# Kernel tuning notes

Hardware: AMD Instinct MI355X
Metric: run time of the kernel (lower is better)

Reference implementation:

```python
import jax, jax.numpy as jnp
import numpy as np

B, N_UNITS, SEQ, H = 4, 1024, 2048, 8
D_HEAD = N_UNITS // H
SCALE = 1.0 / D_HEAD ** 0.5


def setup_inputs() -> dict:
    key = jax.random.key(0)
    k1, k2, k3 = jax.random.split(key, 3)
    x = jax.random.normal(k1, (B, N_UNITS, SEQ), dtype=jnp.float32)
    # conv1x1 weights, bias=False; scaled like typical init
    W_qkv = jax.random.normal(k2, (3 * N_UNITS, N_UNITS), dtype=jnp.float32) * (1.0 / N_UNITS ** 0.5)
    W_out = jax.random.normal(k3, (N_UNITS, N_UNITS), dtype=jnp.float32) * (1.0 / N_UNITS ** 0.5)
    return {"x": x, "W_qkv": W_qkv, "W_out": W_out}


def reference(x, W_qkv, W_out):
    # x: (B, n_units, S). Conv1x1 == per-position linear along channel dim.
    qkv = jnp.einsum('oc,bcs->bos', W_qkv, x)          # (B, 3*n_units, S)
    Q, K, V = jnp.split(qkv, 3, axis=1)                # each (B, n_units, S)
    # torch.chunk along channels into h heads == reshape (B, h, d_head, S)
    Q = Q.reshape(B, H, D_HEAD, SEQ)
    K = K.reshape(B, H, D_HEAD, SEQ)
    V = V.reshape(B, H, D_HEAD, SEQ)
    # scores: Q^T K * scale  (NO softmax in original module; mask unused)
    A = jnp.einsum('bhdq,bhdk->bhqk', Q, K) * SCALE    # (B, h, S, S)
    # aggregation: sum_k A[q,k] * V[d,k]  (original does broadcast mul+sum)
    C = jnp.einsum('bhqk,bhdk->bhdq', A, V)            # (B, h, d_head, S)
    C = C.reshape(B, N_UNITS, SEQ)
    out = jnp.einsum('oc,bcs->bos', W_out, C)          # (B, n_units, S)
    return out
```

## Files before the change

### kernel.cpp

```cpp
#include <hip/hip_runtime.h>
#include <hip/hip_bf16.h>
#include <stdint.h>

using bf16 = __hip_bfloat16;

typedef __bf16 bf16x8 __attribute__((ext_vector_type(8)));
typedef float  f32x4  __attribute__((ext_vector_type(4)));

constexpr int Bc = 4, Hh = 8, Dh = 128, S = 2048, Cn = 1024, O3 = 3072;
constexpr float SCALE = 0.08838834764831845f;

#define GLDS16(gp, lp)                                               \
  __builtin_amdgcn_global_load_lds(                                  \
      (const __attribute__((address_space(1))) void*)(gp),           \
      (__attribute__((address_space(3))) void*)(lp), 16, 0, 0)

#define WAITVM(N) asm volatile("s_waitcnt vmcnt(" #N ")" ::: "memory")
#define BAR()                                  \
  do {                                         \
    asm volatile("" ::: "memory");             \
    __builtin_amdgcn_s_barrier();              \
    asm volatile("" ::: "memory");             \
  } while (0)

__device__ __forceinline__ void gemm_bt_core(
    const bf16* __restrict__ Abase, int lda,
    const bf16* __restrict__ Bbase, int ldb,
    int kIters, f32x4 (&acc)[4][4])
{
  alignas(16) __shared__ bf16 As[128 * 32];
  alignas(16) __shared__ bf16 Bs[128 * 32];
  const int t    = threadIdx.x;
  const int lane = t & 63;
  const int quad = lane >> 4, r16 = lane & 15;
  const int wave = t >> 6;
  const int wm = (wave & 1) * 64, wn = (wave >> 1) * 64;
  const int lrow = lane >> 2;
  const int lk   = (lane & 3) * 8;

  const long aOff0 = (long)(wave * 32 + lrow) * lda + lk;
  const long aOff1 = aOff0 + 16l * lda;
  const long bOff0 = (long)(wave * 32 + lrow) * ldb + lk;
  const long bOff1 = bOff0 + 16l * ldb;
  bf16* aL0 = &As[(wave * 32) * 32];
  bf16* aL1 = &As[(wave * 32 + 16) * 32];
  bf16* bL0 = &Bs[(wave * 32) * 32];
  bf16* bL1 = &Bs[(wave * 32 + 16) * 32];

#pragma unroll
  for (int i = 0; i < 4; i++)
#pragma unroll
    for (int j = 0; j < 4; j++) acc[i][j] = {0.f, 0.f, 0.f, 0.f};

  for (int ks = 0; ks < kIters; ++ks) {
    const int k0 = ks * 32;
    __syncthreads();
    GLDS16(Abase + k0 + aOff0, aL0);
    GLDS16(Abase + k0 + aOff1, aL1);
    GLDS16(Bbase + k0 + bOff0, bL0);
    GLDS16(Bbase + k0 + bOff1, bL1);
    __syncthreads();
    bf16x8 af[4], bfr[4];
#pragma unroll
    for (int i = 0; i < 4; i++)
      af[i] = *(const bf16x8*)&As[(wm + i * 16 + r16) * 32 + quad * 8];
#pragma unroll
    for (int j = 0; j < 4; j++)
      bfr[j] = *(const bf16x8*)&Bs[(wn + j * 16 + r16) * 32 + quad * 8];
#pragma unroll
    for (int i = 0; i < 4; i++)
#pragma unroll
      for (int j = 0; j < 4; j++)
        acc[i][j] = __builtin_amdgcn_mfma_f32_16x16x32_bf16(af[i], bfr[j], acc[i][j], 0, 0, 0);
  }
}

__device__ __forceinline__ void store_bf16_tile(
    f32x4 (&acc)[4][4], bf16* __restrict__ Cp, int ldc)
{
  const int t = threadIdx.x;
  const int lane = t & 63;
  const int quad = lane >> 4, r16 = lane & 15;
  const int wave = t >> 6;
  const int wm = (wave & 1) * 64, wn = (wave >> 1) * 64;
#pragma unroll
  for (int i = 0; i < 4; i++)
#pragma unroll
    for (int j = 0; j < 4; j++)
#pragma unroll
      for (int r = 0; r < 4; r++) {
        const int row = wm + i * 16 + quad * 4 + r;
        const int col = wn + j * 16 + r16;
        Cp[(long)row * ldc + col] = __float2bfloat16(acc[i][j][r]);
      }
}

__device__ __forceinline__ void store_f32_tile(
    f32x4 (&acc)[4][4], float* __restrict__ Cp, int ldc)
{
  const int t = threadIdx.x;
  const int lane = t & 63;
  const int quad = lane >> 4, r16 = lane & 15;
  const int wave = t >> 6;
  const int wm = (wave & 1) * 64, wn = (wave >> 1) * 64;
#pragma unroll
  for (int i = 0; i < 4; i++)
#pragma unroll
    for (int j = 0; j < 4; j++)
#pragma unroll
      for (int r = 0; r < 4; r++) {
        const int row = wm + i * 16 + quad * 4 + r;
        const int col = wn + j * 16 + r16;
        Cp[(long)row * ldc + col] = acc[i][j][r];
      }
}

__device__ __forceinline__ void kv_body(
    const bf16* __restrict__ WkvB, const bf16* __restrict__ xT,
    bf16* __restrict__ KV, bf16* sm, int orig)
{
  constexpr int NT = Cn / 32;
  const int mt = orig >> 5;
  const int nt = ((orig & 7) << 2) | ((orig >> 3) & 3);
  const int m0 = mt * 256;

  const int tid  = threadIdx.x;
  const int lane = tid & 63;
  const int w    = tid >> 6;
  const int quad = lane >> 4, r16 = lane & 15;
  const int wm = (w >> 2) * 128;
  const int wn = (w & 3) * 64;

  const int srow = w * 16 + (lane >> 2);
  const int cx   = (lane & 3) ^ ((lane >> 3) & 3);
  const bf16* Ag = WkvB + (long)(m0 + srow) * Cn + cx * 8;
  const bf16* Bg = xT + (long)((long)nt * 256 + srow) * Cn + cx * 8;
  const int ldsW = w * 512;

#define KV8_STAGE_A(tt)                                                   \
  do {                                                                    \
    const int k0_ = (tt) * 32, bb_ = ((tt) & 3) * 16384;                  \
    GLDS16(Ag + k0_,             &sm[bb_ + ldsW]);                        \
    GLDS16(Ag + 128l * Cn + k0_, &sm[bb_ + 4096 + ldsW]);                 \
  } while (0)
#define KV8_STAGE_B(tt)                                                   \
  do {                                                                    \
    const int k0_ = (tt) * 32, bb_ = ((tt) & 3) * 16384;                  \
    GLDS16(Bg + k0_,             &sm[bb_ + 8192 + ldsW]);                 \
    GLDS16(Bg + 128l * Cn + k0_, &sm[bb_ + 8192 + 4096 + ldsW]);          \
  } while (0)

  const int sc8 = (quad ^ ((r16 >> 1) & 3)) * 8;

  f32x4 acc[8][4];
#pragma unroll
  for (int m = 0; m < 8; m++)
#pragma unroll
    for (int n = 0; n < 4; n++) acc[m][n] = {0.f, 0.f, 0.f, 0.f};

  KV8_STAGE_A(0); KV8_STAGE_B(0);
  KV8_STAGE_A(1); KV8_STAGE_B(1);
  KV8_STAGE_A(2); KV8_STAGE_B(2);
  WAITVM(8);
  BAR();

  bf16x8 af0[4], bfr0[4], af1[4];
  {
    const bf16* Ab = &sm[0];
    const bf16* Bb = Ab + 8192;
#pragma unroll
    for (int n = 0; n < 4; n++)
      bfr0[n] = *(const bf16x8*)&Bb[(wn + n * 16 + r16) * 32 + sc8];
#pragma unroll
    for (int m = 0; m < 4; m++)
      af0[m] = *(const bf16x8*)&Ab[(wm + m * 16 + r16) * 32 + sc8];
  }

#pragma unroll 4
  for (int tt = 0; tt < NT; ++tt) {
    const bf16* Ab = &sm[(tt & 3) * 16384];

    BAR();
    if (tt + 3 < NT) { KV8_STAGE_A(tt + 3); KV8_STAGE_B(tt + 3); }
#pragma unroll
    for (int m = 0; m < 4; m++)
      af1[m] = *(const bf16x8*)&Ab[(wm + (m + 4) * 16 + r16) * 32 + sc8];
    __builtin_amdgcn_s_setprio(1);
#pragma unroll
    for (int m = 0; m < 4; m++)
#pragma unroll
      for (int n = 0; n < 4; n++)
        acc[m][n] = __builtin_amdgcn_mfma_f32_16x16x32_bf16(af0[m], bfr0[n], acc[m][n], 0, 0, 0);
    __builtin_amdgcn_s_setprio(0);

    if (tt <= NT - 4)      { WAITVM(8); }
    else if (tt == NT - 3) { WAITVM(4); }
    else if (tt == NT - 2) { WAITVM(0); }
    BAR();

    __builtin_amdgcn_s_setprio(1);
#pragma unroll
    for (int m = 0; m < 4; m++)
#pragma unroll
      for (int n = 0; n < 4; n++)
        acc[m + 4][n] = __builtin_amdgcn_mfma_f32_16x16x32_bf16(af1[m], bfr0[n], acc[m + 4][n], 0, 0, 0);
    __builtin_amdgcn_s_setprio(0);

    if (tt + 1 < NT) {
      const bf16* Ab2 = &sm[((tt + 1) & 3) * 16384];
      const bf16* Bb2 = Ab2 + 8192;
#pragma unroll
      for (int n = 0; n < 4; n++)
        bfr0[n] = *(const bf16x8*)&Bb2[(wn + n * 16 + r16) * 32 + sc8];
#pragma unroll
      for (int m = 0; m < 4; m++)
        af0[m] = *(const bf16x8*)&Ab2[(wm + m * 16 + r16) * 32 + sc8];
    }
  }

  bf16* Cp = KV + (long)(nt >> 3) * 2048 * S + (long)m0 * S + (nt & 7) * 256;
#pragma unroll
  for (int m = 0; m < 8; m++)
#pragma unroll
    for (int n = 0; n < 4; n++)
#pragma unroll
      for (int r = 0; r < 4; r++) {
        const int row = wm + m * 16 + quad * 4 + r;
        const int col = wn + n * 16 + r16;
        Cp[(long)row * S + col] = __float2bfloat16(acc[m][n][r]);
      }
#undef KV8_STAGE_A
#undef KV8_STAGE_B
}

__device__ __forceinline__ void qt_body(
    const bf16* __restrict__ xT, const bf16* __restrict__ WqB,
    bf16* __restrict__ QT, bf16* sm, int orig)
{
  constexpr int NT = Cn / 32;
  const int b  = orig >> 6;
  const int mt = (orig >> 2) & 15;
  const int nt = orig & 3;
  const int m0 = mt * 128, n0 = nt * 256;

  const int tid  = threadIdx.x;
  const int lane = tid & 63;
  const int w    = tid >> 6;
  const int quad = lane >> 4, r16 = lane & 15;
  const int wm = (w >> 2) * 64;
  const int wn = (w & 3) * 64;

  const int srow = w * 16 + (lane >> 2);
  const int cx   = (lane & 3) ^ ((lane >> 3) & 3);
  const bf16* Ag = xT + (long)b * S * Cn + (long)(m0 + srow) * Cn + cx * 8;
  const bf16* Bg = WqB + (long)(n0 + srow) * Cn + cx * 8;
  const int ldsW = w * 512;

#define QT_STAGE(tt)                                                      \
  do {                                                                    \
    const int k0_ = (tt) * 32, bb_ = ((tt) & 3) * 12288;                  \
    GLDS16(Ag + k0_,             &sm[bb_ + ldsW]);                        \
    GLDS16(Bg + k0_,             &sm[bb_ + 4096 + ldsW]);                 \
    GLDS16(Bg + 128l * Cn + k0_, &sm[bb_ + 8192 + ldsW]);                 \
  } while (0)

  const int sc8 = (quad ^ ((r16 >> 1) & 3)) * 8;

  f32x4 acc[4][4];
#pragma unroll
  for (int m = 0; m < 4; m++)
#pragma unroll
    for (int n = 0; n < 4; n++) acc[m][n] = {0.f, 0.f, 0.f, 0.f};

  QT_STAGE(0); QT_STAGE(1); QT_STAGE(2);
  WAITVM(6);
  BAR();

  bf16x8 af0[2], bfr0[4], af1[2];
  {
    const bf16* Ab = &sm[0];
    const bf16* Bb = Ab + 4096;
#pragma unroll
    for (int n = 0; n < 4; n++)
      bfr0[n] = *(const bf16x8*)&Bb[(wn + n * 16 + r16) * 32 + sc8];
#pragma unroll
    for (int m = 0; m < 2; m++)
      af0[m] = *(const bf16x8*)&Ab[(wm + m * 16 + r16) * 32 + sc8];
  }

#pragma unroll 4
  for (int tt = 0; tt < NT; ++tt) {
    const bf16* Ab = &sm[(tt & 3) * 12288];

    BAR();
    if (tt + 3 < NT) QT_STAGE(tt + 3);
#pragma unroll
    for (int m = 0; m < 2; m++)
      af1[m] = *(const bf16x8*)&Ab[(wm + (m + 2) * 16 + r16) * 32 + sc8];
    __builtin_amdgcn_s_setprio(1);
#pragma unroll
    for (int m = 0; m < 2; m++)
#pragma unroll
      for (int n = 0; n < 4; n++)
        acc[m][n] = __builtin_amdgcn_mfma_f32_16x16x32_bf16(af0[m], bfr0[n], acc[m][n], 0, 0, 0);
    __builtin_amdgcn_s_setprio(0);

    if (tt <= NT - 4)      { WAITVM(6); }
    else if (tt == NT - 3) { WAITVM(3); }
    else if (tt == NT - 2) { WAITVM(0); }
    BAR();

    __builtin_amdgcn_s_setprio(1);
#pragma unroll
    for (int m = 0; m < 2; m++)
#pragma unroll
      for (int n = 0; n < 4; n++)
        acc[m + 2][n] = __builtin_amdgcn_mfma_f32_16x16x32_bf16(af1[m], bfr0[n], acc[m + 2][n], 0, 0, 0);
    __builtin_amdgcn_s_setprio(0);

    if (tt + 1 < NT) {
      const bf16* Ab2 = &sm[((tt + 1) & 3) * 12288];
      const bf16* Bb2 = Ab2 + 4096;
#pragma unroll
      for (int n = 0; n < 4; n++)
        bfr0[n] = *(const bf16x8*)&Bb2[(wn + n * 16 + r16) * 32 + sc8];
#pragma unroll
      for (int m = 0; m < 2; m++)
        af0[m] = *(const bf16x8*)&Ab2[(wm + m * 16 + r16) * 32 + sc8];
    }
  }

  bf16* Cp = QT + (long)b * S * Cn + (long)m0 * Cn + n0;
#pragma unroll
  for (int m = 0; m < 4; m++)
#pragma unroll
    for (int n = 0; n < 4; n++)
#pragma unroll
      for (int r = 0; r < 4; r++) {
        const int row = wm + m * 16 + quad * 4 + r;
        const int col = wn + n * 16 + r16;
        Cp[(long)row * Cn + col] = __float2bfloat16(acc[m][n][r]);
      }
#undef QT_STAGE
}

__global__ __launch_bounds__(512, 2) void k_kvqt8(
    const bf16* __restrict__ WkvB, const bf16* __restrict__ xT,
    bf16* __restrict__ KV, const bf16* __restrict__ WqB, bf16* __restrict__ QT)
{
  alignas(16) __shared__ bf16 smem[4 * 16384];
  const int bid = blockIdx.x;
  if (bid < 256) kv_body(WkvB, xT, KV, smem, bid);
  else           qt_body(xT, WqB, QT, smem, bid - 256);
}

__global__ __launch_bounds__(256) void k_prep(
    const float* __restrict__ x, bf16* __restrict__ xT,
    const float* __restrict__ Wqkv, const float* __restrict__ Wout,
    bf16* __restrict__ WqkvB, bf16* __restrict__ WoutB)
{
  __shared__ bf16 tile[32][33];
  if (blockIdx.z < 4) {
    const float* ip = x + (long)blockIdx.z * 1024 * 2048;
    bf16* op = xT + (long)blockIdx.z * 2048 * 1024;
    const int c0 = blockIdx.x * 32, r0 = blockIdx.y * 32;
    const int tx = threadIdx.x & 31, ty = threadIdx.x >> 5;
#pragma unroll
    for (int i = 0; i < 32; i += 8)
      tile[ty + i][tx] = __float2bfloat16(ip[(long)(r0 + ty + i) * 2048 + c0 + tx]);
    __syncthreads();
#pragma unroll
    for (int i = 0; i < 32; i += 8)
      op[(long)(c0 + ty + i) * 1024 + r0 + tx] = tile[tx][ty + i];
  } else {
    const long blk = (long)blockIdx.x + (long)blockIdx.y * 64;
#pragma unroll
    for (int i = 0; i < 2; i++) {
      const long v = blk * 512 + i * 256 + threadIdx.x;
      const bool isQ = v < 786432;
      const float4 f = isQ ? ((const float4*)Wqkv)[v] : ((const float4*)Wout)[v - 786432];
      bf16 tmp[4];
      tmp[0] = __float2bfloat16(f.x);
      tmp[1] = __float2bfloat16(f.y);
      tmp[2] = __float2bfloat16(f.z);
      tmp[3] = __float2bfloat16(f.w);
      ushort4 u = *(ushort4*)tmp;
      if (isQ) ((ushort4*)WqkvB)[v] = u;
      else     ((ushort4*)WoutB)[v - 786432] = u;
    }
  }
}

__global__ __launch_bounds__(512, 2) void k_gemm_out8(
    const bf16* __restrict__ W2, const bf16* __restrict__ QT, float* __restrict__ out)
{
  constexpr int NT = Cn / 32;
  alignas(16) __shared__ bf16 smem[4 * 12288];

  const int orig = blockIdx.x;
  const int swz  = (orig & 7) * 32 + (orig >> 3);
  const int b  = swz >> 6;
  const int mt = (swz >> 3) & 7;
  const int nt = swz & 7;
  const int m0 = mt * 128, n0 = nt * 256;

  const int tid  = threadIdx.x;
  const int lane = tid & 63;
  const int w    = tid >> 6;
  const int quad = lane >> 4, r16 = lane & 15;
  const int wm = (w >> 2) * 64;
  const int wn = (w & 3) * 64;

  const int srow = w * 16 + (lane >> 2);
  const int cx   = (lane & 3) ^ ((lane >> 3) & 3);
  const bf16* Ag = W2 + (long)b * Cn * Cn + (long)(m0 + srow) * Cn + cx * 8;
  const bf16* Bg = QT + (long)b * S * Cn + (long)(n0 + srow) * Cn + cx * 8;
  const int ldsW = w * 512;

#define OUT_STAGE(tt)                                                     \
  do {                                                                    \
    const int k0_ = (tt) * 32, bb_ = ((tt) & 3) * 12288;                  \
    GLDS16(Ag + k0_,             &smem[bb_ + ldsW]);                      \
    GLDS16(Bg + k0_,             &smem[bb_ + 4096 + ldsW]);               \
    GLDS16(Bg + 128l * Cn + k0_, &smem[bb_ + 8192 + ldsW]);               \
  } while (0)

  const int sc8 = (quad ^ ((r16 >> 1) & 3)) * 8;

  f32x4 acc[4][4];
#pragma unroll
  for (int m = 0; m < 4; m++)
#pragma unroll
    for (int n = 0; n < 4; n++) acc[m][n] = {0.f, 0.f, 0.f, 0.f};

  OUT_STAGE(0); OUT_STAGE(1); OUT_STAGE(2);
  WAITVM(6);
  BAR();

  bf16x8 af0[2], bfr0[4], af1[2];
  {
    const bf16* Ab = &smem[0];
    const bf16* Bb = Ab + 4096;
#pragma unroll
    for (int n = 0; n < 4; n++)
      bfr0[n] = *(const bf16x8*)&Bb[(wn + n * 16 + r16) * 32 + sc8];
#pragma unroll
    for (int m = 0; m < 2; m++)
      af0[m] = *(const bf16x8*)&Ab[(wm + m * 16 + r16) * 32 + sc8];
  }

#pragma unroll 4
  for (int tt = 0; tt < NT; ++tt) {
    const bf16* Ab = &smem[(tt & 3) * 12288];

    BAR();
    if (tt + 3 < NT) OUT_STAGE(tt + 3);
#pragma unroll
    for (int m = 0; m < 2; m++)
      af1[m] = *(const bf16x8*)&Ab[(wm + (m + 2) * 16 + r16) * 32 + sc8];
    __builtin_amdgcn_s_setprio(1);
#pragma unroll
    for (int m = 0; m < 2; m++)
#pragma unroll
      for (int n = 0; n < 4; n++)
        acc[m][n] = __builtin_amdgcn_mfma_f32_16x16x32_bf16(af0[m], bfr0[n], acc[m][n], 0, 0, 0);
    __builtin_amdgcn_s_setprio(0);

    if (tt <= NT - 4)      { WAITVM(6); }
    else if (tt == NT - 3) { WAITVM(3); }
    else if (tt == NT - 2) { WAITVM(0); }
    BAR();

    __builtin_amdgcn_s_setprio(1);
#pragma unroll
    for (int m = 0; m < 2; m++)
#pragma unroll
      for (int n = 0; n < 4; n++)
        acc[m + 2][n] = __builtin_amdgcn_mfma_f32_16x16x32_bf16(af1[m], bfr0[n], acc[m + 2][n], 0, 0, 0);
    __builtin_amdgcn_s_setprio(0);

    if (tt + 1 < NT) {
      const bf16* Ab2 = &smem[((tt + 1) & 3) * 12288];
      const bf16* Bb2 = Ab2 + 4096;
#pragma unroll
      for (int n = 0; n < 4; n++)
        bfr0[n] = *(const bf16x8*)&Bb2[(wn + n * 16 + r16) * 32 + sc8];
#pragma unroll
      for (int m = 0; m < 2; m++)
        af0[m] = *(const bf16x8*)&Ab2[(wm + m * 16 + r16) * 32 + sc8];
    }
  }

  float* Cp = out + (long)b * Cn * S + (long)m0 * S + n0;
#pragma unroll
  for (int m = 0; m < 4; m++)
#pragma unroll
    for (int n = 0; n < 4; n++)
#pragma unroll
      for (int r = 0; r < 4; r++) {
        const int row = wm + m * 16 + quad * 4 + r;
        const int col = wn + n * 16 + r16;
        Cp[(long)row * S + col] = acc[m][n][r];
      }
#undef OUT_STAGE
}

__global__ __launch_bounds__(256) void k_gemm_mt(
    const bf16* __restrict__ KV, float* __restrict__ MTpart)
{
  const int chunk = blockIdx.x;
  const int z = blockIdx.y;
  const int b = z >> 3, h = z & 7;
  const bf16* base = KV + (long)b * 2048 * S;
  const bf16* A  = base + (long)(h * Dh) * S + chunk * 256;
  const bf16* Bp = base + (long)(1024 + h * Dh) * S + chunk * 256;
  f32x4 acc[4][4];
  gemm_bt_core(A, S, Bp, S, 8, acc);
  store_f32_tile(acc, MTpart + ((long)chunk * 32 + z) * (Dh * Dh), Dh);
}

__global__ __launch_bounds__(256) void k_reduce_mt(
    const float* __restrict__ MTpart, bf16* __restrict__ MbT)
{
  const long i = (long)blockIdx.x * 256 + threadIdx.x;
  float s = 0.f;
#pragma unroll
  for (int c = 0; c < 8; c++) s += MTpart[(long)c * 32 * Dh * Dh + i];
  MbT[i] = __float2bfloat16(s * SCALE);
}

__global__ __launch_bounds__(256) void k_gemm_w2(
    const bf16* __restrict__ WoutB, const bf16* __restrict__ MbT, bf16* __restrict__ W2)
{
  const int m0 = blockIdx.x * 128;
  const int h = blockIdx.y, b = blockIdx.z;
  const int z = b * 8 + h;
  f32x4 acc[4][4];
  gemm_bt_core(WoutB + (long)m0 * Cn + h * Dh, Cn,
               MbT + (long)z * Dh * Dh, Dh, 4, acc);
  store_bf16_tile(acc, W2 + (long)b * Cn * Cn + (long)m0 * Cn + h * Dh, Cn);
}

extern "C" void kernel_launch(void* const* d_in, const int* in_sizes, int n_in,
                              void* d_out, int out_size, void* d_ws, size_t ws_size,
                              hipStream_t stream)
{
  const float* x    = (const float*)d_in[0];
  const float* Wqkv = (const float*)d_in[1];
  const float* Wout = (const float*)d_in[2];
  float* out = (float*)d_out;

  char* ws = (char*)d_ws;
  bf16*  KV     = (bf16*)ws;
  bf16*  xT     = (bf16*)(ws + 33554432);
  bf16*  QT     = (bf16*)(ws + 50331648);
  bf16*  WqkvB  = (bf16*)(ws + 67108864);
  bf16*  WoutB  = (bf16*)(ws + 73400320);
  bf16*  MbT    = (bf16*)(ws + 75497472);
  bf16*  W2     = (bf16*)(ws + 76546048);
  bf16*  WkvB   = WqkvB + (long)Cn * Cn;
  float* MTpart = out;

  k_prep<<<dim3(64, 32, 5), 256, 0, stream>>>(x, xT, Wqkv, Wout, WqkvB, WoutB);
  k_kvqt8<<<dim3(512), 512, 0, stream>>>(WkvB, xT, KV, WqkvB, QT);
  k_gemm_mt<<<dim3(8, 32), 256, 0, stream>>>(KV, MTpart);
  k_reduce_mt<<<dim3(2048), 256, 0, stream>>>(MTpart, MbT);
  k_gemm_w2<<<dim3(8, 8, 4), 256, 0, stream>>>(WoutB, MbT, W2);
  k_gemm_out8<<<dim3(256), 512, 0, stream>>>(W2, QT, out);
}
```

Measured before the change: 198.0 us.

## Shrink KV tiles to 256x128 and use 3-stage LDS ring for occupancy

The KV GEMM tile drops from 256x256 to 256x128, so twice as many blocks are launched and each needs fewer accumulators. All three fused GEMM bodies (KV, QT, output) move from a 4-buffer to a 3-buffer LDS ring with rotating pointers, and launch bounds go from 2 to 4 blocks per CU. The goal is higher occupancy and better latency hiding from lower LDS and register use. In exchange the pipeline has a shallower prefetch depth, and the smaller KV tile gives less data reuse per block.

```diff
diff --git a/kernel.cpp b/kernel.cpp
--- a/kernel.cpp
+++ b/kernel.cpp
@@ -115,112 +115,103 @@
       }
 }
 
+
 __device__ __forceinline__ void kv_body(
     const bf16* __restrict__ WkvB, const bf16* __restrict__ xT,
     bf16* __restrict__ KV, bf16* sm, int orig)
 {
   constexpr int NT = Cn / 32;
-  const int mt = orig >> 5;
-  const int nt = ((orig & 7) << 2) | ((orig >> 3) & 3);
+  const int mt = orig >> 6;
+  const int nt = ((orig & 7) << 3) | ((orig >> 3) & 7);
   const int m0 = mt * 256;
 
   const int tid  = threadIdx.x;
   const int lane = tid & 63;
   const int w    = tid >> 6;
   const int quad = lane >> 4, r16 = lane & 15;
-  const int wm = (w >> 2) * 128;
-  const int wn = (w & 3) * 64;
+  const int wm = (w >> 1) * 64;
+  const int wn = (w & 1) * 64;
 
   const int srow = w * 16 + (lane >> 2);
   const int cx   = (lane & 3) ^ ((lane >> 3) & 3);
   const bf16* Ag = WkvB + (long)(m0 + srow) * Cn + cx * 8;
-  const bf16* Bg = xT + (long)((long)nt * 256 + srow) * Cn + cx * 8;
+  const bf16* Bg = xT + (long)((long)nt * 128 + srow) * Cn + cx * 8;
   const int ldsW = w * 512;
 
-#define KV8_STAGE_A(tt)                                                   \
+#define KV_STAGE(base, tt)                                                \
   do {                                                                    \
-    const int k0_ = (tt) * 32, bb_ = ((tt) & 3) * 16384;                  \
-    GLDS16(Ag + k0_,             &sm[bb_ + ldsW]);                        \
-    GLDS16(Ag + 128l * Cn + k0_, &sm[bb_ + 4096 + ldsW]);                 \
+    const int k0_ = (tt) * 32;                                            \
+    GLDS16(Ag + k0_,             (base) + ldsW);                          \
+    GLDS16(Ag + 128l * Cn + k0_, (base) + 4096 + ldsW);                   \
+    GLDS16(Bg + k0_,             (base) + 8192 + ldsW);                   \
   } while (0)
-#define KV8_STAGE_B(tt)                                                   \
-  do {                                                                    \
-    const int k0_ = (tt) * 32, bb_ = ((tt) & 3) * 16384;                  \
-    GLDS16(Bg + k0_,             &sm[bb_ + 8192 + ldsW]);                 \
-    GLDS16(Bg + 128l * Cn + k0_, &sm[bb_ + 8192 + 4096 + ldsW]);          \
-  } while (0)
 
   const int sc8 = (quad ^ ((r16 >> 1) & 3)) * 8;
 
-  f32x4 acc[8][4];
-#pragma unroll
-  for (int m = 0; m < 8; m++)
+  f32x4 acc[4][4];
+#pragma unroll
+  for (int m = 0; m < 4; m++)
 #pragma unroll
     for (int n = 0; n < 4; n++) acc[m][n] = {0.f, 0.f, 0.f, 0.f};
 
-  KV8_STAGE_A(0); KV8_STAGE_B(0);
-  KV8_STAGE_A(1); KV8_STAGE_B(1);
-  KV8_STAGE_A(2); KV8_STAGE_B(2);
-  WAITVM(8);
+  bf16* bufc = sm;
+  bf16* bufn = sm + 12288;
+  bf16* bufs = sm + 24576;
+
+  KV_STAGE(bufc, 0); KV_STAGE(bufn, 1);
+  WAITVM(3);
   BAR();
 
-  bf16x8 af0[4], bfr0[4], af1[4];
-  {
-    const bf16* Ab = &sm[0];
-    const bf16* Bb = Ab + 8192;
-#pragma unroll
-    for (int n = 0; n < 4; n++)
-      bfr0[n] = *(const bf16x8*)&Bb[(wn + n * 16 + r16) * 32 + sc8];
-#pragma unroll
-    for (int m = 0; m < 4; m++)
-      af0[m] = *(const bf16x8*)&Ab[(wm + m * 16 + r16) * 32 + sc8];
-  }
-
-#pragma unroll 4
+  bf16x8 af0[2], af1[2], bfr0[4];
+#pragma unroll
+  for (int n = 0; n < 4; n++)
+    bfr0[n] = *(const bf16x8*)&bufc[8192 + (wn + n * 16 + r16) * 32 + sc8];
+#pragma unroll
+  for (int m = 0; m < 2; m++)
+    af0[m] = *(const bf16x8*)&bufc[(wm + m * 16 + r16) * 32 + sc8];
+
+#pragma unroll 3
   for (int tt = 0; tt < NT; ++tt) {
-    const bf16* Ab = &sm[(tt & 3) * 16384];
-
     BAR();
-    if (tt + 3 < NT) { KV8_STAGE_A(tt + 3); KV8_STAGE_B(tt + 3); }
-#pragma unroll
-    for (int m = 0; m < 4; m++)
-      af1[m] = *(const bf16x8*)&Ab[(wm + (m + 4) * 16 + r16) * 32 + sc8];
+    if (tt + 2 < NT) KV_STAGE(bufs, tt + 2);
+#pragma unroll
+    for (int m = 0; m < 2; m++)
+      af1[m] = *(const bf16x8*)&bufc[(wm + (m + 2) * 16 + r16) * 32 + sc8];
     __builtin_amdgcn_s_setprio(1);
 #pragma unroll
-    for (int m = 0; m < 4; m++)
+    for (int m = 0; m < 2; m++)
 #pragma unroll
       for (int n = 0; n < 4; n++)
         acc[m][n] = __builtin_amdgcn_mfma_f32_16x16x32_bf16(af0[m], bfr0[n], acc[m][n], 0, 0, 0);
     __builtin_amdgcn_s_setprio(0);
 
-    if (tt <= NT - 4)      { WAITVM(8); }
-    else if (tt == NT - 3) { WAITVM(4); }
+    if (tt < NT - 2)       { WAITVM(3); }
     else if (tt == NT - 2) { WAITVM(0); }
     BAR();
 
     __builtin_amdgcn_s_setprio(1);
 #pragma unroll
-    for (int m = 0; m < 4; m++)
-#pragma unroll
-      for (int n = 0; n < 4; n++)
-        acc[m + 4][n] = __builtin_amdgcn_mfma_f32_16x16x32_bf16(af1[m], bfr0[n], acc[m + 4][n], 0, 0, 0);
+    for (int m = 0; m < 2; m++)
+#pragma unroll
+      for (int n = 0; n < 4; n++)
+        acc[m + 2][n] = __builtin_amdgcn_mfma_f32_16x16x32_bf16(af1[m], bfr0[n], acc[m + 2][n], 0, 0, 0);
     __builtin_amdgcn_s_setprio(0);
 
     if (tt + 1 < NT) {
-      const bf16* Ab2 = &sm[((tt + 1) & 3) * 16384];
-      const bf16* Bb2 = Ab2 + 8192;
-#pragma unroll
-      for (int n = 0; n < 4; n++)
-        bfr0[n] = *(const bf16x8*)&Bb2[(wn + n * 16 + r16) * 32 + sc8];
-#pragma unroll
-      for (int m = 0; m < 4; m++)
-        af0[m] = *(const bf16x8*)&Ab2[(wm + m * 16 + r16) * 32 + sc8];
+#pragma unroll
+      for (int n = 0; n < 4; n++)
+        bfr0[n] = *(const bf16x8*)&bufn[8192 + (wn + n * 16 + r16) * 32 + sc8];
+#pragma unroll
+      for (int m = 0; m < 2; m++)
+        af0[m] = *(const bf16x8*)&bufn[(wm + m * 16 + r16) * 32 + sc8];
     }
+    bf16* t_ = bufc; bufc = bufn; bufn = bufs; bufs = t_;
   }
 
-  bf16* Cp = KV + (long)(nt >> 3) * 2048 * S + (long)m0 * S + (nt & 7) * 256;
-#pragma unroll
-  for (int m = 0; m < 8; m++)
+  const int b = nt >> 4, scol = (nt & 15) * 128;
+  bf16* Cp = KV + (long)b * 2048 * S + (long)m0 * S + scol;
+#pragma unroll
+  for (int m = 0; m < 4; m++)
 #pragma unroll
     for (int n = 0; n < 4; n++)
 #pragma unroll
@@ -229,8 +220,7 @@
         const int col = wn + n * 16 + r16;
         Cp[(long)row * S + col] = __float2bfloat16(acc[m][n][r]);
       }
-#undef KV8_STAGE_A
-#undef KV8_STAGE_B
+#undef KV_STAGE
 }
 
 __device__ __forceinline__ void qt_body(
@@ -256,12 +246,12 @@
   const bf16* Bg = WqB + (long)(n0 + srow) * Cn + cx * 8;
   const int ldsW = w * 512;
 
-#define QT_STAGE(tt)                                                      \
+#define QT_STAGE(base, tt)                                                \
   do {                                                                    \
-    const int k0_ = (tt) * 32, bb_ = ((tt) & 3) * 12288;                  \
-    GLDS16(Ag + k0_,             &sm[bb_ + ldsW]);                        \
-    GLDS16(Bg + k0_,             &sm[bb_ + 4096 + ldsW]);                 \
-    GLDS16(Bg + 128l * Cn + k0_, &sm[bb_ + 8192 + ldsW]);                 \
+    const int k0_ = (tt) * 32;                                            \
+    GLDS16(Ag + k0_,             (base) + ldsW);                          \
+    GLDS16(Bg + k0_,             (base) + 4096 + ldsW);                   \
+    GLDS16(Bg + 128l * Cn + k0_, (base) + 8192 + ldsW);                   \
   } while (0)
 
   const int sc8 = (quad ^ ((r16 >> 1) & 3)) * 8;
@@ -272,31 +262,29 @@
 #pragma unroll
     for (int n = 0; n < 4; n++) acc[m][n] = {0.f, 0.f, 0.f, 0.f};
 
-  QT_STAGE(0); QT_STAGE(1); QT_STAGE(2);
-  WAITVM(6);
+  bf16* bufc = sm;
+  bf16* bufn = sm + 12288;
+  bf16* bufs = sm + 24576;
+
+  QT_STAGE(bufc, 0); QT_STAGE(bufn, 1);
+  WAITVM(3);
   BAR();
 
-  bf16x8 af0[2], bfr0[4], af1[2];
-  {
-    const bf16* Ab = &sm[0];
-    const bf16* Bb = Ab + 4096;
-#pragma unroll
-    for (int n = 0; n < 4; n++)
-      bfr0[n] = *(const bf16x8*)&Bb[(wn + n * 16 + r16) * 32 + sc8];
-#pragma unroll
-    for (int m = 0; m < 2; m++)
-      af0[m] = *(const bf16x8*)&Ab[(wm + m * 16 + r16) * 32 + sc8];
-  }
-
-#pragma unroll 4
+  bf16x8 af0[2], af1[2], bfr0[4];
+#pragma unroll
+  for (int n = 0; n < 4; n++)
+    bfr0[n] = *(const bf16x8*)&bufc[4096 + (wn + n * 16 + r16) * 32 + sc8];
+#pragma unroll
+  for (int m = 0; m < 2; m++)
+    af0[m] = *(const bf16x8*)&bufc[(wm + m * 16 + r16) * 32 + sc8];
+
+#pragma unroll 3
   for (int tt = 0; tt < NT; ++tt) {
-    const bf16* Ab = &sm[(tt & 3) * 12288];
-
     BAR();
-    if (tt + 3 < NT) QT_STAGE(tt + 3);
-#pragma unroll
-    for (int m = 0; m < 2; m++)
-      af1[m] = *(const bf16x8*)&Ab[(wm + (m + 2) * 16 + r16) * 32 + sc8];
+    if (tt + 2 < NT) QT_STAGE(bufs, tt + 2);
+#pragma unroll
+    for (int m = 0; m < 2; m++)
+      af1[m] = *(const bf16x8*)&bufc[(wm + (m + 2) * 16 + r16) * 32 + sc8];
     __builtin_amdgcn_s_setprio(1);
 #pragma unroll
     for (int m = 0; m < 2; m++)
@@ -305,8 +293,7 @@
         acc[m][n] = __builtin_amdgcn_mfma_f32_16x16x32_bf16(af0[m], bfr0[n], acc[m][n], 0, 0, 0);
     __builtin_amdgcn_s_setprio(0);
 
-    if (tt <= NT - 4)      { WAITVM(6); }
-    else if (tt == NT - 3) { WAITVM(3); }
+    if (tt < NT - 2)       { WAITVM(3); }
     else if (tt == NT - 2) { WAITVM(0); }
     BAR();
 
@@ -319,15 +306,14 @@
     __builtin_amdgcn_s_setprio(0);
 
     if (tt + 1 < NT) {
-      const bf16* Ab2 = &sm[((tt + 1) & 3) * 12288];
-      const bf16* Bb2 = Ab2 + 4096;
-#pragma unroll
-      for (int n = 0; n < 4; n++)
-        bfr0[n] = *(const bf16x8*)&Bb2[(wn + n * 16 + r16) * 32 + sc8];
+#pragma unroll
+      for (int n = 0; n < 4; n++)
+        bfr0[n] = *(const bf16x8*)&bufn[4096 + (wn + n * 16 + r16) * 32 + sc8];
 #pragma unroll
       for (int m = 0; m < 2; m++)
-        af0[m] = *(const bf16x8*)&Ab2[(wm + m * 16 + r16) * 32 + sc8];
+        af0[m] = *(const bf16x8*)&bufn[(wm + m * 16 + r16) * 32 + sc8];
     }
+    bf16* t_ = bufc; bufc = bufn; bufn = bufs; bufs = t_;
   }
 
   bf16* Cp = QT + (long)b * S * Cn + (long)m0 * Cn + n0;
@@ -344,14 +330,124 @@
 #undef QT_STAGE
 }
 
-__global__ __launch_bounds__(512, 2) void k_kvqt8(
+__global__ __launch_bounds__(512, 4) void k_kvqt8(
     const bf16* __restrict__ WkvB, const bf16* __restrict__ xT,
     bf16* __restrict__ KV, const bf16* __restrict__ WqB, bf16* __restrict__ QT)
 {
-  alignas(16) __shared__ bf16 smem[4 * 16384];
+  alignas(16) __shared__ bf16 smem[3 * 12288];
   const int bid = blockIdx.x;
-  if (bid < 256) kv_body(WkvB, xT, KV, smem, bid);
-  else           qt_body(xT, WqB, QT, smem, bid - 256);
+  if (bid < 512) kv_body(WkvB, xT, KV, smem, bid);
+  else           qt_body(xT, WqB, QT, smem, bid - 512);
+}
+
+__global__ __launch_bounds__(512, 4) void k_gemm_out8(
+    const bf16* __restrict__ W2, const bf16* __restrict__ QT, float* __restrict__ out)
+{
+  constexpr int NT = Cn / 32;
+  alignas(16) __shared__ bf16 smem[3 * 12288];
+
+  const int orig = blockIdx.x;
+  const int swz  = (orig & 7) * 32 + (orig >> 3);
+  const int b  = swz >> 6;
+  const int mt = (swz >> 3) & 7;
+  const int nt = swz & 7;
+  const int m0 = mt * 128, n0 = nt * 256;
+
+  const int tid  = threadIdx.x;
+  const int lane = tid & 63;
+  const int w    = tid >> 6;
+  const int quad = lane >> 4, r16 = lane & 15;
+  const int wm = (w >> 2) * 64;
+  const int wn = (w & 3) * 64;
+
+  const int srow = w * 16 + (lane >> 2);
+  const int cx   = (lane & 3) ^ ((lane >> 3) & 3);
+  const bf16* Ag = W2 + (long)b * Cn * Cn + (long)(m0 + srow) * Cn + cx * 8;
+  const bf16* Bg = QT + (long)b * S * Cn + (long)(n0 + srow) * Cn + cx * 8;
+  const int ldsW = w * 512;
+
+#define OUT_STAGE(base, tt)                                               \
+  do {                                                                    \
+    const int k0_ = (tt) * 32;                                            \
+    GLDS16(Ag + k0_,             (base) + ldsW);                          \
+    GLDS16(Bg + k0_,             (base) + 4096 + ldsW);                   \
+    GLDS16(Bg + 128l * Cn + k0_, (base) + 8192 + ldsW);                   \
+  } while (0)
+
+  const int sc8 = (quad ^ ((r16 >> 1) & 3)) * 8;
+
+  f32x4 acc[4][4];
+#pragma unroll
+  for (int m = 0; m < 4; m++)
+#pragma unroll
+    for (int n = 0; n < 4; n++) acc[m][n] = {0.f, 0.f, 0.f, 0.f};
+
+  bf16* bufc = smem;
+  bf16* bufn = smem + 12288;
+  bf16* bufs = smem + 24576;
+
+  OUT_STAGE(bufc, 0); OUT_STAGE(bufn, 1);
+  WAITVM(3);
+  BAR();
+
+  bf16x8 af0[2], af1[2], bfr0[4];
+#pragma unroll
+  for (int n = 0; n < 4; n++)
+    bfr0[n] = *(const bf16x8*)&bufc[4096 + (wn + n * 16 + r16) * 32 + sc8];
+#pragma unroll
+  for (int m = 0; m < 2; m++)
+    af0[m] = *(const bf16x8*)&bufc[(wm + m * 16 + r16) * 32 + sc8];
+
+#pragma unroll 3
+  for (int tt = 0; tt < NT; ++tt) {
+    BAR();
+    if (tt + 2 < NT) OUT_STAGE(bufs, tt + 2);
+#pragma unroll
+    for (int m = 0; m < 2; m++)
+      af1[m] = *(const bf16x8*)&bufc[(wm + (m + 2) * 16 + r16) * 32 + sc8];
+    __builtin_amdgcn_s_setprio(1);
+#pragma unroll
+    for (int m = 0; m < 2; m++)
+#pragma unroll
+      for (int n = 0; n < 4; n++)
+        acc[m][n] = __builtin_amdgcn_mfma_f32_16x16x32_bf16(af0[m], bfr0[n], acc[m][n], 0, 0, 0);
+    __builtin_amdgcn_s_setprio(0);
+
+    if (tt < NT - 2)       { WAITVM(3); }
+    else if (tt == NT - 2) { WAITVM(0); }
+    BAR();
+
+    __builtin_amdgcn_s_setprio(1);
+#pragma unroll
+    for (int m = 0; m < 2; m++)
+#pragma unroll
+      for (int n = 0; n < 4; n++)
+        acc[m + 2][n] = __builtin_amdgcn_mfma_f32_16x16x32_bf16(af1[m], bfr0[n], acc[m + 2][n], 0, 0, 0);
+    __builtin_amdgcn_s_setprio(0);
+
+    if (tt + 1 < NT) {
+#pragma unroll
+      for (int n = 0; n < 4; n++)
+        bfr0[n] = *(const bf16x8*)&bufn[4096 + (wn + n * 16 + r16) * 32 + sc8];
+#pragma unroll
+      for (int m = 0; m < 2; m++)
+        af0[m] = *(const bf16x8*)&bufn[(wm + m * 16 + r16) * 32 + sc8];
+    }
+    bf16* t_ = bufc; bufc = bufn; bufn = bufs; bufs = t_;
+  }
+
+  float* Cp = out + (long)b * Cn * S + (long)m0 * S + n0;
+#pragma unroll
+  for (int m = 0; m < 4; m++)
+#pragma unroll
+    for (int n = 0; n < 4; n++)
+#pragma unroll
+      for (int r = 0; r < 4; r++) {
+        const int row = wm + m * 16 + quad * 4 + r;
+        const int col = wn + n * 16 + r16;
+        Cp[(long)row * S + col] = acc[m][n][r];
+      }
+#undef OUT_STAGE
 }
 
 __global__ __launch_bounds__(256) void k_prep(
@@ -391,120 +487,6 @@
   }
 }
 
-__global__ __launch_bounds__(512, 2) void k_gemm_out8(
-    const bf16* __restrict__ W2, const bf16* __restrict__ QT, float* __restrict__ out)
-{
-  constexpr int NT = Cn / 32;
-  alignas(16) __shared__ bf16 smem[4 * 12288];
-
-  const int orig = blockIdx.x;
-  const int swz  = (orig & 7) * 32 + (orig >> 3);
-  const int b  = swz >> 6;
-  const int mt = (swz >> 3) & 7;
-  const int nt = swz & 7;
-  const int m0 = mt * 128, n0 = nt * 256;
-
-  const int tid  = threadIdx.x;
-  const int lane = tid & 63;
-  const int w    = tid >> 6;
-  const int quad = lane >> 4, r16 = lane & 15;
-  const int wm = (w >> 2) * 64;
-  const int wn = (w & 3) * 64;
-
-  const int srow = w * 16 + (lane >> 2);
-  const int cx   = (lane & 3) ^ ((lane >> 3) & 3);
-  const bf16* Ag = W2 + (long)b * Cn * Cn + (long)(m0 + srow) * Cn + cx * 8;
-  const bf16* Bg = QT + (long)b * S * Cn + (long)(n0 + srow) * Cn + cx * 8;
-  const int ldsW = w * 512;
-
-#define OUT_STAGE(tt)                                                     \
-  do {                                                                    \
-    const int k0_ = (tt) * 32, bb_ = ((tt) & 3) * 12288;                  \
-    GLDS16(Ag + k0_,             &smem[bb_ + ldsW]);                      \
-    GLDS16(Bg + k0_,             &smem[bb_ + 4096 + ldsW]);               \
-    GLDS16(Bg + 128l * Cn + k0_, &smem[bb_ + 8192 + ldsW]);               \
-  } while (0)
-
-  const int sc8 = (quad ^ ((r16 >> 1) & 3)) * 8;
-
-  f32x4 acc[4][4];
-#pragma unroll
-  for (int m = 0; m < 4; m++)
-#pragma unroll
-    for (int n = 0; n < 4; n++) acc[m][n] = {0.f, 0.f, 0.f, 0.f};
-
-  OUT_STAGE(0); OUT_STAGE(1); OUT_STAGE(2);
-  WAITVM(6);
-  BAR();
-
-  bf16x8 af0[2], bfr0[4], af1[2];
-  {
-    const bf16* Ab = &smem[0];
-    const bf16* Bb = Ab + 4096;
-#pragma unroll
-    for (int n = 0; n < 4; n++)
-      bfr0[n] = *(const bf16x8*)&Bb[(wn + n * 16 + r16) * 32 + sc8];
-#pragma unroll
-    for (int m = 0; m < 2; m++)
-      af0[m] = *(const bf16x8*)&Ab[(wm + m * 16 + r16) * 32 + sc8];
-  }
-
-#pragma unroll 4
-  for (int tt = 0; tt < NT; ++tt) {
-    const bf16* Ab = &smem[(tt & 3) * 12288];
-
-    BAR();
-    if (tt + 3 < NT) OUT_STAGE(tt + 3);
-#pragma unroll
-    for (int m = 0; m < 2; m++)
-      af1[m] = *(const bf16x8*)&Ab[(wm + (m + 2) * 16 + r16) * 32 + sc8];
-    __builtin_amdgcn_s_setprio(1);
-#pragma unroll
-    for (int m = 0; m < 2; m++)
-#pragma unroll
-      for (int n = 0; n < 4; n++)
-        acc[m][n] = __builtin_amdgcn_mfma_f32_16x16x32_bf16(af0[m], bfr0[n], acc[m][n], 0, 0, 0);
-    __builtin_amdgcn_s_setprio(0);
-
-    if (tt <= NT - 4)      { WAITVM(6); }
-    else if (tt == NT - 3) { WAITVM(3); }
-    else if (tt == NT - 2) { WAITVM(0); }
-    BAR();
-
-    __builtin_amdgcn_s_setprio(1);
-#pragma unroll
-    for (int m = 0; m < 2; m++)
-#pragma unroll
-      for (int n = 0; n < 4; n++)
-        acc[m + 2][n] = __builtin_amdgcn_mfma_f32_16x16x32_bf16(af1[m], bfr0[n], acc[m + 2][n], 0, 0, 0);
-    __builtin_amdgcn_s_setprio(0);
-
-    if (tt + 1 < NT) {
-      const bf16* Ab2 = &smem[((tt + 1) & 3) * 12288];
-      const bf16* Bb2 = Ab2 + 4096;
-#pragma unroll
-      for (int n = 0; n < 4; n++)
-        bfr0[n] = *(const bf16x8*)&Bb2[(wn + n * 16 + r16) * 32 + sc8];
-#pragma unroll
-      for (int m = 0; m < 2; m++)
-        af0[m] = *(const bf16x8*)&Ab2[(wm + m * 16 + r16) * 32 + sc8];
-    }
-  }
-
-  float* Cp = out + (long)b * Cn * S + (long)m0 * S + n0;
-#pragma unroll
-  for (int m = 0; m < 4; m++)
-#pragma unroll
-    for (int n = 0; n < 4; n++)
-#pragma unroll
-      for (int r = 0; r < 4; r++) {
-        const int row = wm + m * 16 + quad * 4 + r;
-        const int col = wn + n * 16 + r16;
-        Cp[(long)row * S + col] = acc[m][n][r];
-      }
-#undef OUT_STAGE
-}
-
 __global__ __launch_bounds__(256) void k_gemm_mt(
     const bf16* __restrict__ KV, float* __restrict__ MTpart)
 {
@@ -562,7 +544,7 @@
   float* MTpart = out;
 
   k_prep<<<dim3(64, 32, 5), 256, 0, stream>>>(x, xT, Wqkv, Wout, WqkvB, WoutB);
-  k_kvqt8<<<dim3(512), 512, 0, stream>>>(WkvB, xT, KV, WqkvB, QT);
+  k_kvqt8<<<dim3(768), 512, 0, stream>>>(WkvB, xT, KV, WqkvB, QT);
   k_gemm_mt<<<dim3(8, 32), 256, 0, stream>>>(KV, MTpart);
   k_reduce_mt<<<dim3(2048), 256, 0, stream>>>(MTpart, MbT);
   k_gemm_w2<<<dim3(8, 8, 4), 256, 0, stream>>>(WoutB, MbT, W2);
```

Measured after the change: 196.6 us. Within noise of the previous version (-0.7%).
